# Optimization experiments

Hardware: AMD Instinct MI355X
Metric: run time of the kernel (lower is better)

The kernel has to match this reference:

```python
import jax, jax.numpy as jnp
import numpy as np

B, N, F, E, M, O = 1024, 64, 64, 16, 128, 128
MESSAGE_PASSES = 4


def setup_inputs() -> dict:
    key = jax.random.key(0)
    ks = jax.random.split(key, 10)
    adjacency = jax.random.randint(ks[0], (B, N, N), 0, 2, dtype=jnp.int32)
    adjacency = adjacency * (1 - jnp.eye(N, dtype=jnp.int32))  # no self loops
    nodes = jax.random.normal(ks[1], (B, N, F), dtype=jnp.float32)
    edges = jax.random.normal(ks[2], (B, N, N, E), dtype=jnp.float32)
    s = lambda n: 1.0 / np.sqrt(n)
    W_n = jax.random.normal(ks[3], (F, M), dtype=jnp.float32) * s(F)
    W_e = jax.random.normal(ks[4], (E, M), dtype=jnp.float32) * s(E)
    b_m = jnp.zeros((M,), dtype=jnp.float32)
    W_u = jax.random.normal(ks[5], (F + M, F), dtype=jnp.float32) * s(F + M)
    b_u = jnp.zeros((F,), dtype=jnp.float32)
    W_r = jax.random.normal(ks[6], (2 * F, O), dtype=jnp.float32) * s(2 * F)
    b_r = jnp.zeros((O,), dtype=jnp.float32)
    return {"adjacency": adjacency, "nodes": nodes, "edges": edges,
            "W_n": W_n, "W_e": W_e, "b_m": b_m,
            "W_u": W_u, "b_u": b_u, "W_r": W_r, "b_r": b_r}


def reference(adjacency, nodes, edges, W_n, W_e, b_m, W_u, b_u, W_r, b_r):
    adj = adjacency.astype(nodes.dtype)            # [B,N,N] 0/1 neighbour mask
    node_mask = (adj.sum(-1) > 0)                  # [B,N] nodes with degree > 0
    h = nodes
    for _ in range(MESSAGE_PASSES):
        # masked neighbour aggregation (linear message -> sum-before-project is exact)
        agg_h = jnp.einsum('bvu,buf->bvf', adj, h)       # sum of neighbour hidden states
        agg_e = jnp.einsum('bvu,bvue->bve', adj, edges)  # sum of incident edge features
        msg = agg_h @ W_n + agg_e @ W_e + b_m            # [B,N,M]
        h_new = jax.nn.relu(jnp.concatenate([h, msg], axis=-1) @ W_u + b_u)
        # only nodes present in the graph get updated (matches scatter in torch code)
        h = jnp.where(node_mask[..., None], h_new, h)
    r = jax.nn.relu(jnp.concatenate([h, nodes], axis=-1) @ W_r + b_r)  # [B,N,O]
    out = jnp.sum(r * node_mask[..., None].astype(r.dtype), axis=1)    # [B,O]
    return out
```

## Files before the change

kernel.cpp:

```cpp
#include <hip/hip_runtime.h>
#include <cstdint>
#include <cstddef>

typedef float f32x4 __attribute__((ext_vector_type(4)));
typedef int   i32x4 __attribute__((ext_vector_type(4)));

#define WNU_OFF 0
#define WEU_OFF (64 * 64)
#define BMU_OFF (64 * 64 + 16 * 64)

__global__ __launch_bounds__(64) void prep_kernel(
    const float* __restrict__ W_n, const float* __restrict__ W_e,
    const float* __restrict__ b_m, const float* __restrict__ W_u,
    const float* __restrict__ b_u, float* __restrict__ ws)
{
    const int blk = blockIdx.x, j = threadIdx.x;
    const float* Wu2 = W_u + 64 * 64;
    if (blk < 64) {
        float acc = 0.f;
        for (int k = 0; k < 128; ++k) acc += W_n[blk * 128 + k] * Wu2[k * 64 + j];
        ws[WNU_OFF + blk * 64 + j] = acc;
    } else if (blk < 80) {
        const int e = blk - 64;
        float acc = 0.f;
        for (int k = 0; k < 128; ++k) acc += W_e[e * 128 + k] * Wu2[k * 64 + j];
        ws[WEU_OFF + e * 64 + j] = acc;
    } else {
        float acc = b_u[j];
        for (int k = 0; k < 128; ++k) acc += b_m[k] * Wu2[k * 64 + j];
        ws[BMU_OFF + j] = acc;
    }
}

__global__ __launch_bounds__(256, 3) void mpnn_kernel(
    const int* __restrict__ adjacency, const float* __restrict__ nodes,
    const float* __restrict__ edges, const float* __restrict__ W_u,
    const float* __restrict__ W_r, const float* __restrict__ b_r,
    const float* __restrict__ ws, float* __restrict__ out)
{
    __shared__ __align__(16) float bufA[64 * 68];
    __shared__ __align__(16) float bufB[64 * 68];
    __shared__ unsigned long long maskRow[64];
    __shared__ __align__(16) float scratch[16 * 128];

    const int b  = blockIdx.x;
    const int t  = threadIdx.x;
    const int w  = t >> 6;
    const int l  = t & 63;
    const int rg = t >> 4;
    const int cg = t & 15;

    {
        const i32x4* arow = (const i32x4*)(adjacency + ((size_t)b * 64 + (t >> 2)) * 64 + (t & 3) * 16);
        unsigned m16 = 0;
#pragma unroll
        for (int j = 0; j < 4; ++j) {
            const i32x4 a = __builtin_nontemporal_load(arow + j);
            m16 |= (a.x != 0 ? 1u : 0u) << (4 * j + 0);
            m16 |= (a.y != 0 ? 1u : 0u) << (4 * j + 1);
            m16 |= (a.z != 0 ? 1u : 0u) << (4 * j + 2);
            m16 |= (a.w != 0 ? 1u : 0u) << (4 * j + 3);
        }
        ((unsigned*)scratch)[t] = m16;
    }
    {
        const int v = t >> 2, cb = (t & 3) * 16;
        const float4* np = (const float4*)(nodes + ((size_t)b * 64 + v) * 64 + cb);
        float4* hp = (float4*)&bufA[v * 68 + cb];
#pragma unroll
        for (int cc = 0; cc < 4; ++cc) hp[cc] = np[cc];
    }
    __syncthreads();
    if (t < 64) {
        const unsigned* mp = (const unsigned*)scratch;
        maskRow[t] = (unsigned long long)mp[t * 4 + 0]
                   | ((unsigned long long)mp[t * 4 + 1] << 16)
                   | ((unsigned long long)mp[t * 4 + 2] << 32)
                   | ((unsigned long long)mp[t * 4 + 3] << 48);
    }
    __syncthreads();

    {
        const int vs = l >> 4, us = (l >> 2) & 3, e4 = l & 3;
        float* agge = scratch;
#pragma unroll
        for (int g = 0; g < 4; ++g) {
            const int v = 16 * w + 4 * g + vs;
            const unsigned long long mv = maskRow[v];
            const unsigned mlo = (unsigned)mv, mhi = (unsigned)(mv >> 32);
            const float* ebase = edges + ((size_t)b * 64 + v) * 1024 + us * 16 + e4 * 4;
            float a0 = 0.f, a1 = 0.f, a2 = 0.f, a3 = 0.f;
#pragma unroll
            for (int i = 0; i < 16; ++i) {
                const unsigned mm = (i < 8) ? mlo : mhi;
                const float m = (float)((mm >> ((i * 4) & 31)) >> us & 1u);
                const f32x4 ev = __builtin_nontemporal_load((const f32x4*)(ebase + i * 64));
                a0 += m * ev.x; a1 += m * ev.y; a2 += m * ev.z; a3 += m * ev.w;
            }
#pragma unroll
            for (int off = 4; off <= 8; off <<= 1) {
                a0 += __shfl_xor(a0, off, 64);
                a1 += __shfl_xor(a1, off, 64);
                a2 += __shfl_xor(a2, off, 64);
                a3 += __shfl_xor(a3, off, 64);
            }
            if (us == 0) *(float4*)&agge[v * 20 + e4 * 4] = make_float4(a0, a1, a2, a3);
        }
    }
    __syncthreads();

    unsigned long long mk[4];
    float updf[4];
#pragma unroll
    for (int i = 0; i < 4; ++i) {
        mk[i] = maskRow[rg + 16 * i];
        updf[i] = (mk[i] != 0ULL) ? 1.f : 0.f;
    }

    float msg[4][4];
    {
        const float* Weu = ws + WEU_OFF;
        const float* agge = scratch;
        const float4 bm = *(const float4*)(ws + BMU_OFF + 4 * cg);
#pragma unroll
        for (int i = 0; i < 4; ++i) {
            const int v = rg + 16 * i;
            float m0 = bm.x, m1 = bm.y, m2 = bm.z, m3 = bm.w;
#pragma unroll
            for (int e = 0; e < 16; ++e) {
                const float a = agge[v * 20 + e];
                const float4 wv = *(const float4*)(Weu + e * 64 + 4 * cg);
                m0 += a * wv.x; m1 += a * wv.y; m2 += a * wv.z; m3 += a * wv.w;
            }
            msg[i][0] = m0; msg[i][1] = m1; msg[i][2] = m2; msg[i][3] = m3;
        }
    }
    __syncthreads();

    const float* Wu1 = W_u;
    const float* Wnu = ws + WNU_OFF;
    float* cur = bufA;
    float* oth = bufB;

    for (int pass = 0; pass < 4; ++pass) {
        float s[4][4];
#pragma unroll
        for (int i = 0; i < 4; ++i)
#pragma unroll
            for (int j = 0; j < 4; ++j) s[i][j] = 0.f;
#pragma unroll 1
        for (int half = 0; half < 2; ++half) {
            unsigned mm0 = (unsigned)(mk[0] >> (32 * half));
            unsigned mm1 = (unsigned)(mk[1] >> (32 * half));
            unsigned mm2 = (unsigned)(mk[2] >> (32 * half));
            unsigned mm3 = (unsigned)(mk[3] >> (32 * half));
            const float* hb = cur + (half * 32) * 68 + 4 * cg;
#pragma unroll 8
            for (int uu = 0; uu < 32; ++uu) {
                const float4 hv = *(const float4*)(hb + uu * 68);
                const float f0 = (float)(mm0 & 1u); mm0 >>= 1;
                const float f1 = (float)(mm1 & 1u); mm1 >>= 1;
                const float f2 = (float)(mm2 & 1u); mm2 >>= 1;
                const float f3 = (float)(mm3 & 1u); mm3 >>= 1;
                s[0][0] += f0 * hv.x; s[0][1] += f0 * hv.y; s[0][2] += f0 * hv.z; s[0][3] += f0 * hv.w;
                s[1][0] += f1 * hv.x; s[1][1] += f1 * hv.y; s[1][2] += f1 * hv.z; s[1][3] += f1 * hv.w;
                s[2][0] += f2 * hv.x; s[2][1] += f2 * hv.y; s[2][2] += f2 * hv.z; s[2][3] += f2 * hv.w;
                s[3][0] += f3 * hv.x; s[3][1] += f3 * hv.y; s[3][2] += f3 * hv.z; s[3][3] += f3 * hv.w;
            }
        }
#pragma unroll
        for (int i = 0; i < 4; ++i)
            *(float4*)&oth[(rg + 16 * i) * 68 + 4 * cg] =
                make_float4(s[i][0], s[i][1], s[i][2], s[i][3]);

        float acc[4][4];
#pragma unroll
        for (int i = 0; i < 4; ++i)
#pragma unroll
            for (int j = 0; j < 4; ++j) acc[i][j] = msg[i][j];
#pragma unroll 8
        for (int k = 0; k < 64; ++k) {
            const float4 w1 = *(const float4*)(Wu1 + k * 64 + 4 * cg);
            const float4 w2 = *(const float4*)(Wnu + k * 64 + 4 * cg);
#pragma unroll
            for (int i = 0; i < 4; ++i) {
                const float ah = cur[(rg + 16 * i) * 68 + k];
                const float ag = oth[(rg + 16 * i) * 68 + k];
                acc[i][0] += ah * w1.x + ag * w2.x;
                acc[i][1] += ah * w1.y + ag * w2.y;
                acc[i][2] += ah * w1.z + ag * w2.z;
                acc[i][3] += ah * w1.w + ag * w2.w;
            }
        }
#pragma unroll
        for (int i = 0; i < 4; ++i) {
            const int v = rg + 16 * i;
            const float4 oldv = *(const float4*)&cur[v * 68 + 4 * cg];
            float4 nv;
            nv.x = (mk[i] != 0ULL) ? fmaxf(acc[i][0], 0.f) : oldv.x;
            nv.y = (mk[i] != 0ULL) ? fmaxf(acc[i][1], 0.f) : oldv.y;
            nv.z = (mk[i] != 0ULL) ? fmaxf(acc[i][2], 0.f) : oldv.z;
            nv.w = (mk[i] != 0ULL) ? fmaxf(acc[i][3], 0.f) : oldv.w;
            *(float4*)&oth[v * 68 + 4 * cg] = nv;
        }
        __syncthreads();
        float* tmp = cur; cur = oth; oth = tmp;
    }

#pragma unroll
    for (int i = 0; i < 4; ++i) {
        const int v = rg + 16 * i;
        const float4 nv = *(const float4*)(nodes + ((size_t)b * 64 + v) * 64 + 4 * cg);
        *(float4*)&oth[v * 68 + 4 * cg] = nv;
    }

    float ro[4][8];
    {
        const float4 br0 = *(const float4*)(b_r + 8 * cg);
        const float4 br1 = *(const float4*)(b_r + 8 * cg + 4);
#pragma unroll
        for (int i = 0; i < 4; ++i) {
            ro[i][0] = br0.x; ro[i][1] = br0.y; ro[i][2] = br0.z; ro[i][3] = br0.w;
            ro[i][4] = br1.x; ro[i][5] = br1.y; ro[i][6] = br1.z; ro[i][7] = br1.w;
        }
    }
#pragma unroll 4
    for (int k = 0; k < 64; ++k) {
        const float4 wa = *(const float4*)(W_r + k * 128 + 8 * cg);
        const float4 wb = *(const float4*)(W_r + k * 128 + 8 * cg + 4);
#pragma unroll
        for (int i = 0; i < 4; ++i) {
            const float ah = cur[(rg + 16 * i) * 68 + k];
            ro[i][0] += ah * wa.x; ro[i][1] += ah * wa.y; ro[i][2] += ah * wa.z; ro[i][3] += ah * wa.w;
            ro[i][4] += ah * wb.x; ro[i][5] += ah * wb.y; ro[i][6] += ah * wb.z; ro[i][7] += ah * wb.w;
        }
    }
#pragma unroll 4
    for (int k = 0; k < 64; ++k) {
        const float4 wa = *(const float4*)(W_r + (64 + k) * 128 + 8 * cg);
        const float4 wb = *(const float4*)(W_r + (64 + k) * 128 + 8 * cg + 4);
#pragma unroll
        for (int i = 0; i < 4; ++i) {
            const float an = oth[(rg + 16 * i) * 68 + k];
            ro[i][0] += an * wa.x; ro[i][1] += an * wa.y; ro[i][2] += an * wa.z; ro[i][3] += an * wa.w;
            ro[i][4] += an * wb.x; ro[i][5] += an * wb.y; ro[i][6] += an * wb.z; ro[i][7] += an * wb.w;
        }
    }
    float rs[8];
#pragma unroll
    for (int j = 0; j < 8; ++j) rs[j] = 0.f;
#pragma unroll
    for (int i = 0; i < 4; ++i)
#pragma unroll
        for (int j = 0; j < 8; ++j) rs[j] += updf[i] * fmaxf(ro[i][j], 0.f);

    float* red = scratch;
    *(float4*)&red[rg * 128 + 8 * cg]     = make_float4(rs[0], rs[1], rs[2], rs[3]);
    *(float4*)&red[rg * 128 + 8 * cg + 4] = make_float4(rs[4], rs[5], rs[6], rs[7]);
    __syncthreads();
    if (t < 128) {
        float sum = 0.f;
#pragma unroll
        for (int i = 0; i < 16; ++i) sum += red[i * 128 + t];
        out[(size_t)b * 128 + t] = sum;
    }
}

extern "C" void kernel_launch(void* const* d_in, const int* in_sizes, int n_in,
                              void* d_out, int out_size, void* d_ws, size_t ws_size,
                              hipStream_t stream)
{
    const int*   adjacency = (const int*)  d_in[0];
    const float* nodes     = (const float*)d_in[1];
    const float* edges     = (const float*)d_in[2];
    const float* W_n       = (const float*)d_in[3];
    const float* W_e       = (const float*)d_in[4];
    const float* b_m       = (const float*)d_in[5];
    const float* W_u       = (const float*)d_in[6];
    const float* b_u       = (const float*)d_in[7];
    const float* W_r       = (const float*)d_in[8];
    const float* b_r       = (const float*)d_in[9];
    float* out = (float*)d_out;
    float* ws  = (float*)d_ws;

    prep_kernel<<<81, 64, 0, stream>>>(W_n, W_e, b_m, W_u, b_u, ws);
    mpnn_kernel<<<1024, 256, 0, stream>>>(adjacency, nodes, edges, W_u, W_r, b_r, ws, out);
}
```

Baseline: 548.0 us.

## Alias scratch into bufB, vectorize LDS reads in GEMM loops, raise occupancy

Removes the separate scratch shared array and reuses bufB for the adjacency mask staging, edge aggregates and the final reduction, with an extra barrier added before the reduction reuses bufB. This cuts LDS use per block so launch bounds can request 4 blocks per CU instead of 3. The update and readout GEMM loops now load hidden-state rows as 128-bit LDS vectors covering 4 k-values at a time, replacing scalar per-k loads. Register pressure from holding the vectors, combined with the tighter occupancy target, may cause spills.

```diff
diff --git a/kernel.cpp b/kernel.cpp
--- a/kernel.cpp
+++ b/kernel.cpp
@@ -32,7 +32,7 @@
     }
 }
 
-__global__ __launch_bounds__(256, 3) void mpnn_kernel(
+__global__ __launch_bounds__(256, 4) void mpnn_kernel(
     const int* __restrict__ adjacency, const float* __restrict__ nodes,
     const float* __restrict__ edges, const float* __restrict__ W_u,
     const float* __restrict__ W_r, const float* __restrict__ b_r,
@@ -41,7 +41,6 @@
     __shared__ __align__(16) float bufA[64 * 68];
     __shared__ __align__(16) float bufB[64 * 68];
     __shared__ unsigned long long maskRow[64];
-    __shared__ __align__(16) float scratch[16 * 128];
 
     const int b  = blockIdx.x;
     const int t  = threadIdx.x;
@@ -61,7 +60,7 @@
             m16 |= (a.z != 0 ? 1u : 0u) << (4 * j + 2);
             m16 |= (a.w != 0 ? 1u : 0u) << (4 * j + 3);
         }
-        ((unsigned*)scratch)[t] = m16;
+        ((unsigned*)bufB)[t] = m16;
     }
     {
         const int v = t >> 2, cb = (t & 3) * 16;
@@ -72,7 +71,7 @@
     }
     __syncthreads();
     if (t < 64) {
-        const unsigned* mp = (const unsigned*)scratch;
+        const unsigned* mp = (const unsigned*)bufB;
         maskRow[t] = (unsigned long long)mp[t * 4 + 0]
                    | ((unsigned long long)mp[t * 4 + 1] << 16)
                    | ((unsigned long long)mp[t * 4 + 2] << 32)
@@ -82,7 +81,7 @@
 
     {
         const int vs = l >> 4, us = (l >> 2) & 3, e4 = l & 3;
-        float* agge = scratch;
+        float* agge = bufB;
 #pragma unroll
         for (int g = 0; g < 4; ++g) {
             const int v = 16 * w + 4 * g + vs;
@@ -120,19 +119,21 @@
     float msg[4][4];
     {
         const float* Weu = ws + WEU_OFF;
-        const float* agge = scratch;
-        const float4 bm = *(const float4*)(ws + BMU_OFF + 4 * cg);
+        const f32x4 bm = *(const f32x4*)(ws + BMU_OFF + 4 * cg);
 #pragma unroll
         for (int i = 0; i < 4; ++i) {
             const int v = rg + 16 * i;
-            float m0 = bm.x, m1 = bm.y, m2 = bm.z, m3 = bm.w;
-#pragma unroll
-            for (int e = 0; e < 16; ++e) {
-                const float a = agge[v * 20 + e];
-                const float4 wv = *(const float4*)(Weu + e * 64 + 4 * cg);
-                m0 += a * wv.x; m1 += a * wv.y; m2 += a * wv.z; m3 += a * wv.w;
-            }
-            msg[i][0] = m0; msg[i][1] = m1; msg[i][2] = m2; msg[i][3] = m3;
+            f32x4 m = bm;
+#pragma unroll
+            for (int q = 0; q < 4; ++q) {
+                const f32x4 a4 = *(const f32x4*)&bufB[v * 20 + q * 4];
+#pragma unroll
+                for (int qq = 0; qq < 4; ++qq) {
+                    const f32x4 wv = *(const f32x4*)(Weu + (q * 4 + qq) * 64 + 4 * cg);
+                    m += a4[qq] * wv;
+                }
+            }
+            msg[i][0] = m.x; msg[i][1] = m.y; msg[i][2] = m.z; msg[i][3] = m.w;
         }
     }
     __syncthreads();
@@ -178,18 +179,25 @@
         for (int i = 0; i < 4; ++i)
 #pragma unroll
             for (int j = 0; j < 4; ++j) acc[i][j] = msg[i][j];
-#pragma unroll 8
-        for (int k = 0; k < 64; ++k) {
-            const float4 w1 = *(const float4*)(Wu1 + k * 64 + 4 * cg);
-            const float4 w2 = *(const float4*)(Wnu + k * 64 + 4 * cg);
+#pragma unroll 4
+        for (int kb = 0; kb < 16; ++kb) {
+            f32x4 hq[4], gq[4];
 #pragma unroll
             for (int i = 0; i < 4; ++i) {
-                const float ah = cur[(rg + 16 * i) * 68 + k];
-                const float ag = oth[(rg + 16 * i) * 68 + k];
-                acc[i][0] += ah * w1.x + ag * w2.x;
-                acc[i][1] += ah * w1.y + ag * w2.y;
-                acc[i][2] += ah * w1.z + ag * w2.z;
-                acc[i][3] += ah * w1.w + ag * w2.w;
+                hq[i] = *(const f32x4*)&cur[(rg + 16 * i) * 68 + 4 * kb];
+                gq[i] = *(const f32x4*)&oth[(rg + 16 * i) * 68 + 4 * kb];
+            }
+#pragma unroll
+            for (int kk = 0; kk < 4; ++kk) {
+                const f32x4 w1 = *(const f32x4*)(Wu1 + (4 * kb + kk) * 64 + 4 * cg);
+                const f32x4 w2 = *(const f32x4*)(Wnu + (4 * kb + kk) * 64 + 4 * cg);
+#pragma unroll
+                for (int i = 0; i < 4; ++i) {
+                    acc[i][0] += hq[i][kk] * w1.x + gq[i][kk] * w2.x;
+                    acc[i][1] += hq[i][kk] * w1.y + gq[i][kk] * w2.y;
+                    acc[i][2] += hq[i][kk] * w1.z + gq[i][kk] * w2.z;
+                    acc[i][3] += hq[i][kk] * w1.w + gq[i][kk] * w2.w;
+                }
             }
         }
 #pragma unroll
@@ -216,34 +224,50 @@
 
     float ro[4][8];
     {
-        const float4 br0 = *(const float4*)(b_r + 8 * cg);
-        const float4 br1 = *(const float4*)(b_r + 8 * cg + 4);
+        const f32x4 br0 = *(const f32x4*)(b_r + 8 * cg);
+        const f32x4 br1 = *(const f32x4*)(b_r + 8 * cg + 4);
 #pragma unroll
         for (int i = 0; i < 4; ++i) {
             ro[i][0] = br0.x; ro[i][1] = br0.y; ro[i][2] = br0.z; ro[i][3] = br0.w;
             ro[i][4] = br1.x; ro[i][5] = br1.y; ro[i][6] = br1.z; ro[i][7] = br1.w;
         }
     }
-#pragma unroll 4
-    for (int k = 0; k < 64; ++k) {
-        const float4 wa = *(const float4*)(W_r + k * 128 + 8 * cg);
-        const float4 wb = *(const float4*)(W_r + k * 128 + 8 * cg + 4);
-#pragma unroll
-        for (int i = 0; i < 4; ++i) {
-            const float ah = cur[(rg + 16 * i) * 68 + k];
-            ro[i][0] += ah * wa.x; ro[i][1] += ah * wa.y; ro[i][2] += ah * wa.z; ro[i][3] += ah * wa.w;
-            ro[i][4] += ah * wb.x; ro[i][5] += ah * wb.y; ro[i][6] += ah * wb.z; ro[i][7] += ah * wb.w;
-        }
-    }
-#pragma unroll 4
-    for (int k = 0; k < 64; ++k) {
-        const float4 wa = *(const float4*)(W_r + (64 + k) * 128 + 8 * cg);
-        const float4 wb = *(const float4*)(W_r + (64 + k) * 128 + 8 * cg + 4);
-#pragma unroll
-        for (int i = 0; i < 4; ++i) {
-            const float an = oth[(rg + 16 * i) * 68 + k];
-            ro[i][0] += an * wa.x; ro[i][1] += an * wa.y; ro[i][2] += an * wa.z; ro[i][3] += an * wa.w;
-            ro[i][4] += an * wb.x; ro[i][5] += an * wb.y; ro[i][6] += an * wb.z; ro[i][7] += an * wb.w;
+#pragma unroll 2
+    for (int kb = 0; kb < 16; ++kb) {
+        f32x4 hq[4];
+#pragma unroll
+        for (int i = 0; i < 4; ++i)
+            hq[i] = *(const f32x4*)&cur[(rg + 16 * i) * 68 + 4 * kb];
+#pragma unroll
+        for (int kk = 0; kk < 4; ++kk) {
+            const f32x4 wa = *(const f32x4*)(W_r + (4 * kb + kk) * 128 + 8 * cg);
+            const f32x4 wb = *(const f32x4*)(W_r + (4 * kb + kk) * 128 + 8 * cg + 4);
+#pragma unroll
+            for (int i = 0; i < 4; ++i) {
+                ro[i][0] += hq[i][kk] * wa.x; ro[i][1] += hq[i][kk] * wa.y;
+                ro[i][2] += hq[i][kk] * wa.z; ro[i][3] += hq[i][kk] * wa.w;
+                ro[i][4] += hq[i][kk] * wb.x; ro[i][5] += hq[i][kk] * wb.y;
+                ro[i][6] += hq[i][kk] * wb.z; ro[i][7] += hq[i][kk] * wb.w;
+            }
+        }
+    }
+#pragma unroll 2
+    for (int kb = 0; kb < 16; ++kb) {
+        f32x4 nq[4];
+#pragma unroll
+        for (int i = 0; i < 4; ++i)
+            nq[i] = *(const f32x4*)&oth[(rg + 16 * i) * 68 + 4 * kb];
+#pragma unroll
+        for (int kk = 0; kk < 4; ++kk) {
+            const f32x4 wa = *(const f32x4*)(W_r + (64 + 4 * kb + kk) * 128 + 8 * cg);
+            const f32x4 wb = *(const f32x4*)(W_r + (64 + 4 * kb + kk) * 128 + 8 * cg + 4);
+#pragma unroll
+            for (int i = 0; i < 4; ++i) {
+                ro[i][0] += nq[i][kk] * wa.x; ro[i][1] += nq[i][kk] * wa.y;
+                ro[i][2] += nq[i][kk] * wa.z; ro[i][3] += nq[i][kk] * wa.w;
+                ro[i][4] += nq[i][kk] * wb.x; ro[i][5] += nq[i][kk] * wb.y;
+                ro[i][6] += nq[i][kk] * wb.z; ro[i][7] += nq[i][kk] * wb.w;
+            }
         }
     }
     float rs[8];
@@ -254,7 +278,8 @@
 #pragma unroll
         for (int j = 0; j < 8; ++j) rs[j] += updf[i] * fmaxf(ro[i][j], 0.f);
 
-    float* red = scratch;
+    __syncthreads();
+    float* red = bufB;
     *(float4*)&red[rg * 128 + 8 * cg]     = make_float4(rs[0], rs[1], rs[2], rs[3]);
     *(float4*)&red[rg * 128 + 8 * cg + 4] = make_float4(rs[4], rs[5], rs[6], rs[7]);
     __syncthreads();
```

New measurement: 511.1 us. 1.07x faster.
